# Kernel optimization log

Hardware: AMD Instinct MI355X
Metric: run time of the kernel (lower is better)

## Reference

```python
import jax, jax.numpy as jnp
import numpy as np

DIM = 768
N_HEADS = 12
HEAD_DIM = DIM // N_HEADS
B, S = 16, 1024


def setup_inputs() -> dict:
    key = jax.random.key(0)
    k1, k2, k3, k4, k5 = jax.random.split(key, 5)
    scale = 0.02
    return {
        "x": jax.random.normal(k1, (B, S, DIM), dtype=jnp.float32),
        "W_attn": jax.random.normal(k2, (DIM, 3 * DIM), dtype=jnp.float32) * scale,
        "b_attn": jnp.zeros((3 * DIM,), dtype=jnp.float32),
        "W_proj": jax.random.normal(k3, (DIM, DIM), dtype=jnp.float32) * scale,
        "b_proj": jnp.zeros((DIM,), dtype=jnp.float32),
    }


def reference(x, W_attn, b_attn, W_proj, b_proj):
    # Dropout layers act as identity (eval mode) for a deterministic reference.
    Bsz, Sq, D = x.shape
    qkv = x @ W_attn + b_attn                      # [B, S, 3D]
    q, k, v = jnp.split(qkv, 3, axis=-1)
    q = q.reshape(Bsz, Sq, N_HEADS, HEAD_DIM)
    k = k.reshape(Bsz, Sq, N_HEADS, HEAD_DIM)
    v = v.reshape(Bsz, Sq, N_HEADS, HEAD_DIM)
    # scores: [B, H, S, S]
    w = jnp.einsum('bqhd,bkhd->bhqk', q, k) / jnp.sqrt(jnp.float32(HEAD_DIM))
    causal = jnp.tril(jnp.ones((Sq, Sq), dtype=bool))
    mask_value = jnp.finfo(w.dtype).min
    w = jnp.where(causal[None, None], w, mask_value)
    w = jax.nn.softmax(w, axis=-1)
    attn = jnp.einsum('bhqk,bkhd->bqhd', w, v).reshape(Bsz, Sq, D)
    return attn @ W_proj + b_proj
```

## Files before the change

kernel.cpp:

```cpp
#include <hip/hip_runtime.h>
#include <hip/hip_bf16.h>
#include <math.h>

#define BDIM 16
#define SEQ 1024
#define DIM 768
#define NH 12
#define HD 64
#define M_ROWS (BDIM * SEQ)
#define N_QKV (3 * DIM)
#define QN (BDIM * NH * SEQ * HD)

typedef __attribute__((ext_vector_type(8))) short bf16x8_t;
typedef __attribute__((ext_vector_type(4))) float f32x4_t;

__device__ __forceinline__ unsigned short f2bf(float x) {
    return __builtin_bit_cast(unsigned short, __float2bfloat16(x));
}

__device__ __forceinline__ void gld_lds16(const void* g, void* l) {
    __builtin_amdgcn_global_load_lds(
        (const __attribute__((address_space(1))) void*)g,
        (__attribute__((address_space(3))) void*)l, 16, 0, 0);
}

#define QSCALE 0.18033688011112042f

#define X_BLOCKS 6144
#define WA_TILES 432
#define WP_TILES 144

__global__ __launch_bounds__(256) void prep(
    const float* __restrict__ x, const float* __restrict__ Wa,
    const float* __restrict__ Wp,
    unsigned short* __restrict__ xb, unsigned short* __restrict__ Wat,
    unsigned short* __restrict__ Wpt)
{
    __shared__ unsigned short T[64][72];
    const int bid = blockIdx.x;
    const int tid = threadIdx.x;

    if (bid < X_BLOCKS) {
        size_t base = (size_t)bid * 2048 + tid * 8;
        float4 f0 = *(const float4*)&x[base];
        float4 f1 = *(const float4*)&x[base + 4];
        unsigned short tmp[8] = {f2bf(f0.x), f2bf(f0.y), f2bf(f0.z), f2bf(f0.w),
                                 f2bf(f1.x), f2bf(f1.y), f2bf(f1.z), f2bf(f1.w)};
        *(uint4*)&xb[base] = *(uint4*)tmp;
        return;
    }
    const float* W; unsigned short* Wt; int N, kt, nt;
    int b2 = bid - X_BLOCKS;
    if (b2 < WA_TILES) { W = Wa; Wt = Wat; N = N_QKV; kt = b2 / 36; nt = b2 % 36; }
    else { b2 -= WA_TILES; W = Wp; Wt = Wpt; N = DIM; kt = b2 / 12; nt = b2 % 12; }
    const int k0 = kt * 64, n0 = nt * 64;
#pragma unroll
    for (int c = 0; c < 4; c++) {
        int idx = c * 256 + tid;
        int r = idx >> 4;
        int c4 = (idx & 15) * 4;
        float4 v = *(const float4*)&W[(size_t)(k0 + r) * N + n0 + c4];
        T[r][c4 + 0] = f2bf(v.x);
        T[r][c4 + 1] = f2bf(v.y);
        T[r][c4 + 2] = f2bf(v.z);
        T[r][c4 + 3] = f2bf(v.w);
    }
    __syncthreads();
#pragma unroll
    for (int c = 0; c < 2; c++) {
        int idx = c * 256 + tid;
        int n = idx >> 3;
        int ch = (idx & 7) * 8;
        unsigned short tmp[8];
#pragma unroll
        for (int j = 0; j < 8; j++) tmp[j] = T[ch + j][n];
        *(uint4*)&Wt[(size_t)(n0 + n) * DIM + k0 + ch] = *(uint4*)tmp;
    }
}

__global__ __launch_bounds__(256, 2) void gemm_qkv_mfma(
    const unsigned short* __restrict__ Ab,
    const unsigned short* __restrict__ Bt,
    const float* __restrict__ bias,
    unsigned short* __restrict__ Qo, unsigned short* __restrict__ Ko,
    unsigned short* __restrict__ Vt)
{
    __shared__ unsigned short smem[32768];

    const int tid = threadIdx.x;
    const int lane = tid & 63;
    const int w = tid >> 6;
    const int wm = w >> 1, wn = w & 1;
    const int ln = lane & 15, quad = lane >> 4;
    const int bm = blockIdx.y * 128, bn = blockIdx.x * 128;

    f32x4_t acc[4][4];
#pragma unroll
    for (int i = 0; i < 4; i++)
#pragma unroll
        for (int j = 0; j < 4; j++) acc[i][j] = (f32x4_t){0.f, 0.f, 0.f, 0.f};

#pragma unroll
    for (int c = 0; c < 4; c++) {
        int idx = c * 256 + tid;
        int r = idx >> 3;
        int gch = (idx & 7) ^ (r & 7);
        gld_lds16(&Ab[(size_t)(bm + r) * DIM + gch * 8], &smem[idx * 8]);
        gld_lds16(&Bt[(size_t)(bn + r) * DIM + gch * 8], &smem[8192 + idx * 8]);
    }

    for (int ki = 0; ki < 12; ki++) {
        __syncthreads();
        unsigned short* As = smem + (ki & 1) * 16384;
        unsigned short* Bs = As + 8192;

        if (ki < 11) {
            const int nk0 = (ki + 1) * 64;
            unsigned short* Asn = smem + ((ki + 1) & 1) * 16384;
            unsigned short* Bsn = Asn + 8192;
#pragma unroll
            for (int c = 0; c < 4; c++) {
                int idx = c * 256 + tid;
                int r = idx >> 3;
                int gch = (idx & 7) ^ (r & 7);
                gld_lds16(&Ab[(size_t)(bm + r) * DIM + nk0 + gch * 8], &Asn[idx * 8]);
                gld_lds16(&Bt[(size_t)(bn + r) * DIM + nk0 + gch * 8], &Bsn[idx * 8]);
            }
        }

#pragma unroll
        for (int kk = 0; kk < 2; kk++) {
            bf16x8_t af[4], bfr[4];
#pragma unroll
            for (int mt = 0; mt < 4; mt++) {
                int r = wm * 64 + mt * 16 + ln;
                int c = (kk * 4 + quad) ^ (ln & 7);
                af[mt] = *(const bf16x8_t*)&As[r * 64 + c * 8];
            }
#pragma unroll
            for (int nt = 0; nt < 4; nt++) {
                int r = wn * 64 + nt * 16 + ln;
                int c = (kk * 4 + quad) ^ (ln & 7);
                bfr[nt] = *(const bf16x8_t*)&Bs[r * 64 + c * 8];
            }
#pragma unroll
            for (int mt = 0; mt < 4; mt++)
#pragma unroll
                for (int nt = 0; nt < 4; nt++)
                    acc[mt][nt] = __builtin_amdgcn_mfma_f32_16x16x32_bf16(
                        af[mt], bfr[nt], acc[mt][nt], 0, 0, 0);
        }
    }
    __syncthreads();

    const int nb = bn + wn * 64;
    const int part = nb / DIM;
    const int h = (nb % DIM) >> 6;
    const float scale = (part == 0) ? QSCALE : 1.0f;
    const int mb = bm + wm * 64;
    const int b_ = mb >> 10;
    const int s0 = mb & 1023;
    unsigned short* Wb = smem + w * 4608;

    float bias_v[4];
#pragma unroll
    for (int nt = 0; nt < 4; nt++) bias_v[nt] = bias[nb + nt * 16 + ln];

    if (part < 2) {
#pragma unroll
        for (int mt = 0; mt < 4; mt++)
#pragma unroll
            for (int nt = 0; nt < 4; nt++)
#pragma unroll
                for (int r = 0; r < 4; r++)
                    Wb[(mt * 16 + quad * 4 + r) * 72 + nt * 16 + ln] =
                        f2bf((acc[mt][nt][r] + bias_v[nt]) * scale);
        unsigned short* dst = (part == 0) ? Qo : Ko;
        size_t obase = (((size_t)b_ * NH + h) * SEQ + s0) * HD;
#pragma unroll
        for (int c = 0; c < 8; c++) {
            int idx = c * 64 + lane;
            int rr = idx >> 3;
            int ch = (idx & 7) * 8;
            *(uint4*)&dst[obase + (size_t)rr * HD + ch] = *(uint4*)&Wb[rr * 72 + ch];
        }
    } else {
#pragma unroll
        for (int mt = 0; mt < 4; mt++)
#pragma unroll
            for (int nt = 0; nt < 4; nt++)
#pragma unroll
                for (int r = 0; r < 4; r++)
                    Wb[(nt * 16 + ln) * 72 + mt * 16 + quad * 4 + r] =
                        f2bf(acc[mt][nt][r] + bias_v[nt]);
        size_t obase = ((size_t)b_ * NH + h) * (size_t)HD * SEQ;
#pragma unroll
        for (int c = 0; c < 8; c++) {
            int idx = c * 64 + lane;
            int d = idx >> 3;
            int ch = (idx & 7) * 8;
            *(uint4*)&Vt[obase + (size_t)d * SEQ + s0 + ch] = *(uint4*)&Wb[d * 72 + ch];
        }
    }
}

__global__ __launch_bounds__(256, 2) void gemm_proj_mfma(
    const unsigned short* __restrict__ Ab,
    const unsigned short* __restrict__ Bt,
    const float* __restrict__ bias,
    float* __restrict__ C)
{
    __shared__ unsigned short smem[32768];

    const int tid = threadIdx.x;
    const int lane = tid & 63;
    const int w = tid >> 6;
    const int wm = w >> 1, wn = w & 1;
    const int ln = lane & 15, quad = lane >> 4;
    const int bm = blockIdx.y * 128, bn = blockIdx.x * 128;

    f32x4_t acc[4][4];
#pragma unroll
    for (int i = 0; i < 4; i++)
#pragma unroll
        for (int j = 0; j < 4; j++) acc[i][j] = (f32x4_t){0.f, 0.f, 0.f, 0.f};

#pragma unroll
    for (int c = 0; c < 4; c++) {
        int idx = c * 256 + tid;
        int r = idx >> 3;
        int gch = (idx & 7) ^ (r & 7);
        gld_lds16(&Ab[(size_t)(bm + r) * DIM + gch * 8], &smem[idx * 8]);
        gld_lds16(&Bt[(size_t)(bn + r) * DIM + gch * 8], &smem[8192 + idx * 8]);
    }

    for (int ki = 0; ki < 12; ki++) {
        __syncthreads();
        unsigned short* As = smem + (ki & 1) * 16384;
        unsigned short* Bs = As + 8192;

        if (ki < 11) {
            const int nk0 = (ki + 1) * 64;
            unsigned short* Asn = smem + ((ki + 1) & 1) * 16384;
            unsigned short* Bsn = Asn + 8192;
#pragma unroll
            for (int c = 0; c < 4; c++) {
                int idx = c * 256 + tid;
                int r = idx >> 3;
                int gch = (idx & 7) ^ (r & 7);
                gld_lds16(&Ab[(size_t)(bm + r) * DIM + nk0 + gch * 8], &Asn[idx * 8]);
                gld_lds16(&Bt[(size_t)(bn + r) * DIM + nk0 + gch * 8], &Bsn[idx * 8]);
            }
        }

#pragma unroll
        for (int kk = 0; kk < 2; kk++) {
            bf16x8_t af[4], bfr[4];
#pragma unroll
            for (int mt = 0; mt < 4; mt++) {
                int r = wm * 64 + mt * 16 + ln;
                int c = (kk * 4 + quad) ^ (ln & 7);
                af[mt] = *(const bf16x8_t*)&As[r * 64 + c * 8];
            }
#pragma unroll
            for (int nt = 0; nt < 4; nt++) {
                int r = wn * 64 + nt * 16 + ln;
                int c = (kk * 4 + quad) ^ (ln & 7);
                bfr[nt] = *(const bf16x8_t*)&Bs[r * 64 + c * 8];
            }
#pragma unroll
            for (int mt = 0; mt < 4; mt++)
#pragma unroll
                for (int nt = 0; nt < 4; nt++)
                    acc[mt][nt] = __builtin_amdgcn_mfma_f32_16x16x32_bf16(
                        af[mt], bfr[nt], acc[mt][nt], 0, 0, 0);
        }
    }

    const int nb = bn + wn * 64;
    float bias_v[4];
#pragma unroll
    for (int nt = 0; nt < 4; nt++) bias_v[nt] = bias[nb + nt * 16 + ln];
#pragma unroll
    for (int mt = 0; mt < 4; mt++)
#pragma unroll
        for (int nt = 0; nt < 4; nt++)
#pragma unroll
            for (int r = 0; r < 4; r++) {
                int m = bm + wm * 64 + mt * 16 + quad * 4 + r;
                C[(size_t)m * DIM + nb + nt * 16 + ln] = acc[mt][nt][r] + bias_v[nt];
            }
}

__global__ __launch_bounds__(256, 3) void attn_mfma(
    const unsigned short* __restrict__ Qg, const unsigned short* __restrict__ Kg,
    const unsigned short* __restrict__ Vt, unsigned short* __restrict__ Out)
{
    __shared__ unsigned short Ks[2][4096];
    __shared__ unsigned short Vs[2][4096];
    __shared__ unsigned short Ps[4][2048];

    const int tid = threadIdx.x;
    const int lane = tid & 63;
    const int w = tid >> 6;
    const int ln = lane & 15;
    const int quad = lane >> 4;
    const int lnx = lane & 7;

    const int bh = blockIdx.y;
    const size_t gbase = (size_t)bh * SEQ * HD;
    const int b_ = bh / NH;
    const int h = bh % NH;

    const int srow = lane >> 3;
    const int scg = (lane & 7) ^ srow;

    for (int ph = 0; ph < 2; ph++) {
        const int qt = ph ? blockIdx.x : 7 - blockIdx.x;
        const int qbase = qt * 128;
        const int ntiles = 2 * qt + 2;

        bf16x8_t aq[2][2];
#pragma unroll
        for (int rg = 0; rg < 2; rg++)
#pragma unroll
            for (int p = 0; p < 2; p++)
                aq[rg][p] = *(const bf16x8_t*)
                    &Qg[gbase + (size_t)(qbase + w * 32 + rg * 16 + ln) * HD +
                        p * 32 + quad * 8];

        float l_r[2][4];
        f32x4_t acc_o[2][4];
#pragma unroll
        for (int rg = 0; rg < 2; rg++)
#pragma unroll
            for (int r = 0; r < 4; r++) {
                l_r[rg][r] = 0.f;
                acc_o[rg][r] = (f32x4_t){0.f, 0.f, 0.f, 0.f};
            }

        __syncthreads();

#pragma unroll
        for (int i = 0; i < 2; i++) {
            int s8 = w * 2 + i;
            int r = s8 * 8 + srow;
            gld_lds16(&Kg[gbase + (size_t)r * HD + scg * 8], &Ks[0][s8 * 512]);
            gld_lds16(&Vt[gbase + (size_t)r * SEQ + scg * 8], &Vs[0][s8 * 512]);
        }

        for (int t = 0; t < ntiles; t++) {
            const int k0 = t * 64;
            const int cur = t & 1;
            __syncthreads();

            if (t + 1 < ntiles) {
                const int nk0 = k0 + 64;
                const int nxt = cur ^ 1;
#pragma unroll
                for (int i = 0; i < 2; i++) {
                    int s8 = w * 2 + i;
                    int r = s8 * 8 + srow;
                    gld_lds16(&Kg[gbase + (size_t)(nk0 + r) * HD + scg * 8],
                              &Ks[nxt][s8 * 512]);
                    gld_lds16(&Vt[gbase + (size_t)r * SEQ + nk0 + scg * 8],
                              &Vs[nxt][s8 * 512]);
                }
            }

            f32x4_t s_acc[2][4];
#pragma unroll
            for (int ct = 0; ct < 4; ct++) {
                bf16x8_t bk0 = *(const bf16x8_t*)
                    &Ks[cur][(ct * 16 + ln) * 64 + ((0 + quad) ^ lnx) * 8];
                bf16x8_t bk1 = *(const bf16x8_t*)
                    &Ks[cur][(ct * 16 + ln) * 64 + ((4 + quad) ^ lnx) * 8];
#pragma unroll
                for (int rg = 0; rg < 2; rg++) {
                    f32x4_t s = (f32x4_t){0.f, 0.f, 0.f, 0.f};
                    s = __builtin_amdgcn_mfma_f32_16x16x32_bf16(aq[rg][0], bk0, s, 0, 0, 0);
                    s = __builtin_amdgcn_mfma_f32_16x16x32_bf16(aq[rg][1], bk1, s, 0, 0, 0);
                    s_acc[rg][ct] = s;
                }
            }

            const bool diag = (t >= 2 * qt);
#pragma unroll
            for (int rg = 0; rg < 2; rg++) {
                const int qrow = qbase + w * 32 + rg * 16 + quad * 4;
#pragma unroll
                for (int ct = 0; ct < 4; ct++) {
                    const int key = k0 + ct * 16 + ln;
#pragma unroll
                    for (int r = 0; r < 4; r++) {
                        float p = exp2f(s_acc[rg][ct][r]);
                        if (diag && key > qrow + r) p = 0.f;
                        s_acc[rg][ct][r] = p;
                        l_r[rg][r] += p;
                    }
                }
            }

#pragma unroll
            for (int rg = 0; rg < 2; rg++)
#pragma unroll
                for (int ct = 0; ct < 4; ct++)
#pragma unroll
                    for (int r = 0; r < 4; r++) {
                        int row = rg * 16 + quad * 4 + r;
                        int pc = (ct * 2 + (ln >> 3)) ^ (row & 7);
                        Ps[w][row * 64 + pc * 8 + lnx] = f2bf(s_acc[rg][ct][r]);
                    }

            bf16x8_t ap[2][2];
#pragma unroll
            for (int rg = 0; rg < 2; rg++)
#pragma unroll
                for (int p = 0; p < 2; p++)
                    ap[rg][p] = *(const bf16x8_t*)
                        &Ps[w][(rg * 16 + ln) * 64 + (((p * 4 + quad) ^ lnx)) * 8];

#pragma unroll
            for (int dt = 0; dt < 4; dt++) {
                bf16x8_t bv0 = *(const bf16x8_t*)
                    &Vs[cur][(dt * 16 + ln) * 64 + ((0 + quad) ^ lnx) * 8];
                bf16x8_t bv1 = *(const bf16x8_t*)
                    &Vs[cur][(dt * 16 + ln) * 64 + ((4 + quad) ^ lnx) * 8];
#pragma unroll
                for (int rg = 0; rg < 2; rg++) {
                    acc_o[rg][dt] = __builtin_amdgcn_mfma_f32_16x16x32_bf16(
                        ap[rg][0], bv0, acc_o[rg][dt], 0, 0, 0);
                    acc_o[rg][dt] = __builtin_amdgcn_mfma_f32_16x16x32_bf16(
                        ap[rg][1], bv1, acc_o[rg][dt], 0, 0, 0);
                }
            }
        }

#pragma unroll
        for (int off = 1; off < 16; off <<= 1)
#pragma unroll
            for (int rg = 0; rg < 2; rg++)
#pragma unroll
                for (int r = 0; r < 4; r++)
                    l_r[rg][r] += __shfl_xor(l_r[rg][r], off);

#pragma unroll
        for (int rg = 0; rg < 2; rg++) {
            float rinv[4];
#pragma unroll
            for (int r = 0; r < 4; r++) rinv[r] = 1.0f / l_r[rg][r];
#pragma unroll
            for (int dt = 0; dt < 4; dt++)
#pragma unroll
                for (int r = 0; r < 4; r++) {
                    int row = qbase + w * 32 + rg * 16 + quad * 4 + r;
                    Out[((size_t)b_ * SEQ + row) * DIM + h * HD + dt * 16 + ln] =
                        f2bf(acc_o[rg][dt][r] * rinv[r]);
                }
        }
    }
}

extern "C" void kernel_launch(void* const* d_in, const int* in_sizes, int n_in,
                              void* d_out, int out_size, void* d_ws, size_t ws_size,
                              hipStream_t stream) {
    const float* x  = (const float*)d_in[0];
    const float* Wa = (const float*)d_in[1];
    const float* ba = (const float*)d_in[2];
    const float* Wp = (const float*)d_in[3];
    const float* bp = (const float*)d_in[4];
    float* out = (float*)d_out;

    unsigned short* ws = (unsigned short*)d_ws;
    unsigned short* Qg  = ws;
    unsigned short* Kg  = Qg + (size_t)QN;
    unsigned short* Vt  = Kg + (size_t)QN;
    unsigned short* xb  = Vt + (size_t)QN;
    unsigned short* AO  = xb + (size_t)QN;
    unsigned short* Wat = AO + (size_t)QN;
    unsigned short* Wpt = Wat + (size_t)(N_QKV * DIM);

    prep<<<X_BLOCKS + WA_TILES + WP_TILES, 256, 0, stream>>>(
        x, Wa, Wp, xb, Wat, Wpt);

    dim3 g_qkv(N_QKV / 128, M_ROWS / 128);
    gemm_qkv_mfma<<<g_qkv, 256, 0, stream>>>(xb, Wat, ba, Qg, Kg, Vt);

    dim3 g_attn(4, BDIM * NH);
    attn_mfma<<<g_attn, 256, 0, stream>>>(Qg, Kg, Vt, AO);

    dim3 g_proj(DIM / 128, M_ROWS / 128);
    gemm_proj_mfma<<<g_proj, 256, 0, stream>>>(AO, Wpt, bp, out);
}
```

Measured before the change: 273.3 us.

## Rewrite attention with 32x32 MFMA, register-resident P via permlane swap, 2-wave blocks

Restructures the attention kernel to use 32x32x16 bf16 MFMA with two waves per block, each wave owning 64 query rows. The S tile is computed transposed (K as A operand), so the probabilities can be packed to bf16 and rearranged in registers with permlane32 swaps instead of a round trip through a shared-memory P buffer. Waves skip key tiles beyond their causal limit, which drops most of the masked work on the diagonal. In exchange, each block has half as many waves to share the K/V loads and hide latency, and register pressure rises from the larger accumulators.

New measurement: 299.3 us. +9.5%, slower.

```diff
diff --git a/kernel.cpp b/kernel.cpp
--- a/kernel.cpp
+++ b/kernel.cpp
@@ -13,6 +13,8 @@
 
 typedef __attribute__((ext_vector_type(8))) short bf16x8_t;
 typedef __attribute__((ext_vector_type(4))) float f32x4_t;
+typedef __attribute__((ext_vector_type(16))) float f32x16_t;
+typedef __attribute__((ext_vector_type(4))) unsigned int u32x4_t;
 
 __device__ __forceinline__ unsigned short f2bf(float x) {
     return __builtin_bit_cast(unsigned short, __float2bfloat16(x));
@@ -22,6 +24,16 @@
     __builtin_amdgcn_global_load_lds(
         (const __attribute__((address_space(1))) void*)g,
         (__attribute__((address_space(3))) void*)l, 16, 0, 0);
+}
+
+__device__ __forceinline__ unsigned int cvt_pk_bf16(float a, float b) {
+    unsigned int r;
+    asm("v_cvt_pk_bf16_f32 %0, %1, %2" : "=v"(r) : "v"(a), "v"(b));
+    return r;
+}
+
+__device__ __forceinline__ void perm32swap(unsigned int& a, unsigned int& b) {
+    asm("v_permlane32_swap_b32 %0, %1" : "+v"(a), "+v"(b));
 }
 
 #define QSCALE 0.18033688011112042f
@@ -292,170 +304,164 @@
             }
 }
 
-__global__ __launch_bounds__(256, 3) void attn_mfma(
+__global__ __launch_bounds__(128, 2) void attn_mfma(
     const unsigned short* __restrict__ Qg, const unsigned short* __restrict__ Kg,
     const unsigned short* __restrict__ Vt, unsigned short* __restrict__ Out)
 {
     __shared__ unsigned short Ks[2][4096];
     __shared__ unsigned short Vs[2][4096];
-    __shared__ unsigned short Ps[4][2048];
 
     const int tid = threadIdx.x;
     const int lane = tid & 63;
     const int w = tid >> 6;
-    const int ln = lane & 15;
-    const int quad = lane >> 4;
-    const int lnx = lane & 7;
+    const int l31 = lane & 31;
+    const int hi = lane >> 5;
+    const int l7 = lane & 7;
 
     const int bh = blockIdx.y;
     const size_t gbase = (size_t)bh * SEQ * HD;
     const int b_ = bh / NH;
     const int h = bh % NH;
 
-    const int srow = lane >> 3;
-    const int scg = (lane & 7) ^ srow;
-
     for (int ph = 0; ph < 2; ph++) {
         const int qt = ph ? blockIdx.x : 7 - blockIdx.x;
         const int qbase = qt * 128;
         const int ntiles = 2 * qt + 2;
-
-        bf16x8_t aq[2][2];
-#pragma unroll
-        for (int rg = 0; rg < 2; rg++)
-#pragma unroll
-            for (int p = 0; p < 2; p++)
-                aq[rg][p] = *(const bf16x8_t*)
-                    &Qg[gbase + (size_t)(qbase + w * 32 + rg * 16 + ln) * HD +
-                        p * 32 + quad * 8];
-
-        float l_r[2][4];
-        f32x4_t acc_o[2][4];
-#pragma unroll
-        for (int rg = 0; rg < 2; rg++)
-#pragma unroll
-            for (int r = 0; r < 4; r++) {
-                l_r[rg][r] = 0.f;
-                acc_o[rg][r] = (f32x4_t){0.f, 0.f, 0.f, 0.f};
-            }
+        const int wtiles = 2 * qt + 1 + w;
+        const int qrow0 = qbase + w * 64;
+
+        bf16x8_t aq[2][4];
+#pragma unroll
+        for (int qg = 0; qg < 2; qg++)
+#pragma unroll
+            for (int ds = 0; ds < 4; ds++)
+                aq[qg][ds] = *(const bf16x8_t*)
+                    &Qg[gbase + (size_t)(qrow0 + qg * 32 + l31) * HD + ds * 16 + hi * 8];
+
+        f32x16_t acc[2][2];
+#pragma unroll
+        for (int qg = 0; qg < 2; qg++)
+#pragma unroll
+            for (int dh = 0; dh < 2; dh++)
+#pragma unroll
+                for (int j = 0; j < 16; j++) acc[qg][dh][j] = 0.f;
+        float lsum[2] = {0.f, 0.f};
 
         __syncthreads();
 
 #pragma unroll
-        for (int i = 0; i < 2; i++) {
-            int s8 = w * 2 + i;
-            int r = s8 * 8 + srow;
-            gld_lds16(&Kg[gbase + (size_t)r * HD + scg * 8], &Ks[0][s8 * 512]);
-            gld_lds16(&Vt[gbase + (size_t)r * SEQ + scg * 8], &Vs[0][s8 * 512]);
+        for (int i = 0; i < 4; i++) {
+            int idx = i * 128 + tid;
+            int r = idx >> 3;
+            int gc = (idx & 7) ^ (r & 7);
+            gld_lds16(&Kg[gbase + (size_t)r * HD + gc * 8], &Ks[0][idx * 8]);
+            gld_lds16(&Vt[gbase + (size_t)r * SEQ + gc * 8], &Vs[0][idx * 8]);
         }
 
         for (int t = 0; t < ntiles; t++) {
-            const int k0 = t * 64;
+            __syncthreads();
             const int cur = t & 1;
-            __syncthreads();
 
             if (t + 1 < ntiles) {
-                const int nk0 = k0 + 64;
-                const int nxt = cur ^ 1;
-#pragma unroll
-                for (int i = 0; i < 2; i++) {
-                    int s8 = w * 2 + i;
-                    int r = s8 * 8 + srow;
-                    gld_lds16(&Kg[gbase + (size_t)(nk0 + r) * HD + scg * 8],
-                              &Ks[nxt][s8 * 512]);
-                    gld_lds16(&Vt[gbase + (size_t)r * SEQ + nk0 + scg * 8],
-                              &Vs[nxt][s8 * 512]);
+                const int nk0 = (t + 1) * 64;
+#pragma unroll
+                for (int i = 0; i < 4; i++) {
+                    int idx = i * 128 + tid;
+                    int r = idx >> 3;
+                    int gc = (idx & 7) ^ (r & 7);
+                    gld_lds16(&Kg[gbase + (size_t)(nk0 + r) * HD + gc * 8],
+                              &Ks[cur ^ 1][idx * 8]);
+                    gld_lds16(&Vt[gbase + (size_t)r * SEQ + nk0 + gc * 8],
+                              &Vs[cur ^ 1][idx * 8]);
                 }
             }
-
-            f32x4_t s_acc[2][4];
-#pragma unroll
-            for (int ct = 0; ct < 4; ct++) {
-                bf16x8_t bk0 = *(const bf16x8_t*)
-                    &Ks[cur][(ct * 16 + ln) * 64 + ((0 + quad) ^ lnx) * 8];
-                bf16x8_t bk1 = *(const bf16x8_t*)
-                    &Ks[cur][(ct * 16 + ln) * 64 + ((4 + quad) ^ lnx) * 8];
-#pragma unroll
-                for (int rg = 0; rg < 2; rg++) {
-                    f32x4_t s = (f32x4_t){0.f, 0.f, 0.f, 0.f};
-                    s = __builtin_amdgcn_mfma_f32_16x16x32_bf16(aq[rg][0], bk0, s, 0, 0, 0);
-                    s = __builtin_amdgcn_mfma_f32_16x16x32_bf16(aq[rg][1], bk1, s, 0, 0, 0);
-                    s_acc[rg][ct] = s;
+            if (t >= wtiles) continue;
+            const bool diag = (t == 2 * qt + w);
+
+#pragma unroll
+            for (int kg = 0; kg < 2; kg++) {
+                bf16x8_t kf[4];
+#pragma unroll
+                for (int ds = 0; ds < 4; ds++)
+                    kf[ds] = *(const bf16x8_t*)
+                        &Ks[cur][(kg * 32 + l31) * 64 + (((ds * 2 + hi) ^ l7) * 8)];
+
+                f32x16_t sa[2];
+#pragma unroll
+                for (int qg = 0; qg < 2; qg++) {
+#pragma unroll
+                    for (int j = 0; j < 16; j++) sa[qg][j] = 0.f;
+#pragma unroll
+                    for (int ds = 0; ds < 4; ds++)
+                        sa[qg] = __builtin_amdgcn_mfma_f32_32x32x16_bf16(
+                            kf[ds], aq[qg][ds], sa[qg], 0, 0, 0);
                 }
-            }
-
-            const bool diag = (t >= 2 * qt);
-#pragma unroll
-            for (int rg = 0; rg < 2; rg++) {
-                const int qrow = qbase + w * 32 + rg * 16 + quad * 4;
-#pragma unroll
-                for (int ct = 0; ct < 4; ct++) {
-                    const int key = k0 + ct * 16 + ln;
-#pragma unroll
-                    for (int r = 0; r < 4; r++) {
-                        float p = exp2f(s_acc[rg][ct][r]);
-                        if (diag && key > qrow + r) p = 0.f;
-                        s_acc[rg][ct][r] = p;
-                        l_r[rg][r] += p;
+
+                bf16x8_t pa[2][2];
+#pragma unroll
+                for (int qg = 0; qg < 2; qg++) {
+                    const int qr = qrow0 + qg * 32 + l31;
+                    float p[16];
+#pragma unroll
+                    for (int j = 0; j < 16; j++) {
+                        float pv = exp2f(sa[qg][j]);
+                        if (diag) {
+                            int key = t * 64 + kg * 32 + (j & 3) + 8 * (j >> 2) + 4 * hi;
+                            if (key > qr) pv = 0.f;
+                        }
+                        lsum[qg] += pv;
+                        p[j] = pv;
                     }
+                    unsigned int c0 = cvt_pk_bf16(p[0], p[1]);
+                    unsigned int c1 = cvt_pk_bf16(p[2], p[3]);
+                    unsigned int c2 = cvt_pk_bf16(p[4], p[5]);
+                    unsigned int c3 = cvt_pk_bf16(p[6], p[7]);
+                    unsigned int c4 = cvt_pk_bf16(p[8], p[9]);
+                    unsigned int c5 = cvt_pk_bf16(p[10], p[11]);
+                    unsigned int c6 = cvt_pk_bf16(p[12], p[13]);
+                    unsigned int c7 = cvt_pk_bf16(p[14], p[15]);
+                    perm32swap(c0, c2);
+                    perm32swap(c1, c3);
+                    perm32swap(c4, c6);
+                    perm32swap(c5, c7);
+                    u32x4_t u0, u1;
+                    u0[0] = c0; u0[1] = c1; u0[2] = c2; u0[3] = c3;
+                    u1[0] = c4; u1[1] = c5; u1[2] = c6; u1[3] = c7;
+                    pa[qg][0] = __builtin_bit_cast(bf16x8_t, u0);
+                    pa[qg][1] = __builtin_bit_cast(bf16x8_t, u1);
                 }
-            }
-
-#pragma unroll
-            for (int rg = 0; rg < 2; rg++)
-#pragma unroll
-                for (int ct = 0; ct < 4; ct++)
-#pragma unroll
-                    for (int r = 0; r < 4; r++) {
-                        int row = rg * 16 + quad * 4 + r;
-                        int pc = (ct * 2 + (ln >> 3)) ^ (row & 7);
-                        Ps[w][row * 64 + pc * 8 + lnx] = f2bf(s_acc[rg][ct][r]);
+
+#pragma unroll
+                for (int ks = 0; ks < 2; ks++)
+#pragma unroll
+                    for (int dh = 0; dh < 2; dh++) {
+                        bf16x8_t vf = *(const bf16x8_t*)
+                            &Vs[cur][(dh * 32 + l31) * 64 +
+                                     (((kg * 4 + ks * 2 + hi) ^ l7) * 8)];
+#pragma unroll
+                        for (int qg = 0; qg < 2; qg++)
+                            acc[qg][dh] = __builtin_amdgcn_mfma_f32_32x32x16_bf16(
+                                pa[qg][ks], vf, acc[qg][dh], 0, 0, 0);
                     }
-
-            bf16x8_t ap[2][2];
-#pragma unroll
-            for (int rg = 0; rg < 2; rg++)
-#pragma unroll
-                for (int p = 0; p < 2; p++)
-                    ap[rg][p] = *(const bf16x8_t*)
-                        &Ps[w][(rg * 16 + ln) * 64 + (((p * 4 + quad) ^ lnx)) * 8];
-
-#pragma unroll
-            for (int dt = 0; dt < 4; dt++) {
-                bf16x8_t bv0 = *(const bf16x8_t*)
-                    &Vs[cur][(dt * 16 + ln) * 64 + ((0 + quad) ^ lnx) * 8];
-                bf16x8_t bv1 = *(const bf16x8_t*)
-                    &Vs[cur][(dt * 16 + ln) * 64 + ((4 + quad) ^ lnx) * 8];
-#pragma unroll
-                for (int rg = 0; rg < 2; rg++) {
-                    acc_o[rg][dt] = __builtin_amdgcn_mfma_f32_16x16x32_bf16(
-                        ap[rg][0], bv0, acc_o[rg][dt], 0, 0, 0);
-                    acc_o[rg][dt] = __builtin_amdgcn_mfma_f32_16x16x32_bf16(
-                        ap[rg][1], bv1, acc_o[rg][dt], 0, 0, 0);
-                }
-            }
-        }
-
-#pragma unroll
-        for (int off = 1; off < 16; off <<= 1)
-#pragma unroll
-            for (int rg = 0; rg < 2; rg++)
-#pragma unroll
-                for (int r = 0; r < 4; r++)
-                    l_r[rg][r] += __shfl_xor(l_r[rg][r], off);
-
-#pragma unroll
-        for (int rg = 0; rg < 2; rg++) {
-            float rinv[4];
-#pragma unroll
-            for (int r = 0; r < 4; r++) rinv[r] = 1.0f / l_r[rg][r];
-#pragma unroll
-            for (int dt = 0; dt < 4; dt++)
-#pragma unroll
-                for (int r = 0; r < 4; r++) {
-                    int row = qbase + w * 32 + rg * 16 + quad * 4 + r;
-                    Out[((size_t)b_ * SEQ + row) * DIM + h * HD + dt * 16 + ln] =
-                        f2bf(acc_o[rg][dt][r] * rinv[r]);
+            }
+        }
+
+        lsum[0] += __shfl_xor(lsum[0], 32);
+        lsum[1] += __shfl_xor(lsum[1], 32);
+
+#pragma unroll
+        for (int qg = 0; qg < 2; qg++) {
+            float rin[16];
+#pragma unroll
+            for (int j = 0; j < 16; j++)
+                rin[j] = 1.0f / __shfl(lsum[qg], (j & 3) + 8 * (j >> 2) + 4 * hi);
+#pragma unroll
+            for (int dh = 0; dh < 2; dh++)
+#pragma unroll
+                for (int j = 0; j < 16; j++) {
+                    int row = qrow0 + qg * 32 + (j & 3) + 8 * (j >> 2) + 4 * hi;
+                    Out[((size_t)b_ * SEQ + row) * DIM + h * HD + dh * 32 + l31] =
+                        f2bf(acc[qg][dh][j] * rin[j]);
                 }
         }
     }
@@ -487,7 +493,7 @@
     gemm_qkv_mfma<<<g_qkv, 256, 0, stream>>>(xb, Wat, ba, Qg, Kg, Vt);
 
     dim3 g_attn(4, BDIM * NH);
-    attn_mfma<<<g_attn, 256, 0, stream>>>(Qg, Kg, Vt, AO);
+    attn_mfma<<<g_attn, 128, 0, stream>>>(Qg, Kg, Vt, AO);
 
     dim3 g_proj(DIM / 128, M_ROWS / 128);
     gemm_proj_mfma<<<g_proj, 256, 0, stream>>>(AO, Wpt, bp, out);
```
